# Performance work log

Measured on AMD Instinct MI355X. Metric: run time of the kernel, lower is better.

The kernel has to match this reference:

```python
import jax, jax.numpy as jnp
import numpy as np

M_CONST = 0.05  # monotonicity margin m from __init__ default


def setup_inputs() -> dict:
    key = jax.random.key(0)
    ks = jax.random.split(key, 5)
    B, IN, OUT = 262144, 128, 128
    scale = 1.0 / np.sqrt(IN)
    return {
        "x": jax.random.normal(ks[0], (B, IN), dtype=jnp.float32),
        "z": jax.random.normal(ks[1], (B, OUT), dtype=jnp.float32),
        "U_w": jax.random.normal(ks[2], (OUT, IN), dtype=jnp.float32) * scale,
        "U_b": jax.random.normal(ks[3], (OUT,), dtype=jnp.float32) * scale,
        "A_w": jax.random.normal(ks[4], (OUT, OUT), dtype=jnp.float32) * scale,
        "d": jnp.zeros((OUT,), dtype=jnp.float32),
    }


def reference(x, z, U_w, U_b, A_w, d):
    # U(x) = x @ U_w.T + U_b
    ux = x @ U_w.T + U_b
    # rowSums diag: diag(|A| @ 1) -> per-output-row abs row sums; z @ diag(r) = z * r
    row_sums = jnp.sum(jnp.abs(A_w), axis=1)  # [OUT]
    dw = jnp.exp(d)                            # diag weights
    # transformedA = diag(1/dw) @ A @ diag(dw); z @ transformedA.T = ((z*dw) @ A.T) * (1/dw)
    z_lin = ((z * dw) @ A_w.T) / dw
    z_out = M_CONST * z + z_lin - z * row_sums
    return (ux + z_out,)
```

## Files before the change

### kernel.cpp

```cpp
#include <hip/hip_runtime.h>
#include <hip/hip_bf16.h>

typedef __attribute__((ext_vector_type(4))) float  f4;
typedef __attribute__((ext_vector_type(4))) float  f32x4;
typedef __attribute__((ext_vector_type(8))) short  bf8;
typedef __attribute__((ext_vector_type(4))) short  s4;

__device__ __forceinline__ short f2bf(float f) {
    unsigned u = __builtin_bit_cast(unsigned, f);
    u += 0x7fff + ((u >> 16) & 1);
    return (short)(u >> 16);
}

__global__ void nemon_prep(const float* __restrict__ Uw,
                           const float* __restrict__ Aw,
                           const float* __restrict__ dvec,
                           short* __restrict__ pre)
{
    __shared__ float rs[128], dwv[128];
    const int tid = threadIdx.x;
    if (tid < 128) {
        float s = 0.f;
        #pragma unroll 8
        for (int k = 0; k < 128; ++k) s += fabsf(Aw[tid * 128 + k]);
        rs[tid]  = s;
        dwv[tid] = expf(dvec[tid]);
    }
    __syncthreads();
    for (int e = tid; e < 32768; e += 256) {
        const int j    = e & 7;
        const int lane = (e >> 3) & 63;
        const int tnt  = e >> 9;
        const int nt   = tnt & 7;
        const int t    = tnt >> 3;
        const int k    = t * 32 + (lane >> 4) * 8 + j;
        const int n    = nt * 16 + (lane & 15);
        float v;
        if (k < 128) {
            v = Uw[n * 128 + k];
        } else {
            const int k2 = k - 128;
            v = Aw[n * 128 + k2] * (dwv[k2] / dwv[n]);
            if (n == k2) v += 0.05f - rs[n];
        }
        pre[e] = f2bf(v);
    }
}

__global__ __launch_bounds__(256, 3) void nemon_main(
    const float* __restrict__ x,
    const float* __restrict__ z,
    const float* __restrict__ Ub,
    const short* __restrict__ pre,
    float* __restrict__ out,
    int ntiles)
{
    __shared__ char S[16384];
    const int tid  = threadIdx.x;
    const int wave = tid >> 6;
    const int lane = tid & 63;
    const int mrow = lane & 15;
    const int kgrp = lane >> 4;

    bf8 wreg[8][2];
    #pragma unroll
    for (int kt = 0; kt < 8; ++kt) {
        #pragma unroll
        for (int j = 0; j < 2; ++j)
            wreg[kt][j] = *(const bf8*)&pre[((kt * 8 + (2 * wave + j)) * 64 + lane) * 8];
    }
    const float ub0 = Ub[(2 * wave)     * 16 + mrow];
    const float ub1 = Ub[(2 * wave + 1) * 16 + mrow];

    for (int tile = blockIdx.x; tile < ntiles; tile += gridDim.x) {
        const long base = (long)tile * 4096;

        f4 xv[4], zv[4];
        #pragma unroll
        for (int i = 0; i < 4; ++i) xv[i] = *(const f4*)(x + base + (tid + i * 256) * 4);
        #pragma unroll
        for (int i = 0; i < 4; ++i) zv[i] = *(const f4*)(z + base + (tid + i * 256) * 4);

        __syncthreads();

        #pragma unroll
        for (int i = 0; i < 4; ++i) {
            const int c   = tid + i * 256;
            const int row = c >> 5;
            const int k2  = (c & 31) * 8;
            const int swz = (row & 7) << 4;
            s4 px = { f2bf(xv[i][0]), f2bf(xv[i][1]), f2bf(xv[i][2]), f2bf(xv[i][3]) };
            s4 pz = { f2bf(zv[i][0]), f2bf(zv[i][1]), f2bf(zv[i][2]), f2bf(zv[i][3]) };
            *(s4*)(S + row * 512 + ( k2         ^ swz)) = px;
            *(s4*)(S + row * 512 + ((k2 + 256)  ^ swz)) = pz;
        }
        __syncthreads();

        f32x4 acc[2][2];
        acc[0][0] = (f32x4){ub0, ub0, ub0, ub0};
        acc[1][0] = acc[0][0];
        acc[0][1] = (f32x4){ub1, ub1, ub1, ub1};
        acc[1][1] = acc[0][1];
        #pragma unroll
        for (int m2 = 0; m2 < 2; ++m2) {
            const int row   = m2 * 16 + mrow;
            const int rbase = row * 512;
            const int swz   = (row & 7) << 4;
            #pragma unroll
            for (int kt = 0; kt < 8; ++kt) {
                bf8 a = *(const bf8*)(S + rbase + ((kt * 64 + kgrp * 16) ^ swz));
                acc[m2][0] = __builtin_amdgcn_mfma_f32_16x16x32_bf16(a, wreg[kt][0], acc[m2][0], 0, 0, 0);
                acc[m2][1] = __builtin_amdgcn_mfma_f32_16x16x32_bf16(a, wreg[kt][1], acc[m2][1], 0, 0, 0);
            }
        }
        __syncthreads();

        float* SF = (float*)S;
        #pragma unroll
        for (int m2 = 0; m2 < 2; ++m2) {
            #pragma unroll
            for (int j2 = 0; j2 < 2; ++j2) {
                #pragma unroll
                for (int jj = 0; jj < 4; ++jj)
                    SF[(m2 * 16 + kgrp * 4 + jj) * 128 + (2 * wave + j2) * 16 + mrow] = acc[m2][j2][jj];
            }
        }
        __syncthreads();

        #pragma unroll
        for (int i = 0; i < 4; ++i) {
            f4 v = *(const f4*)(S + (tid + i * 256) * 16);
            *(f4*)(out + base + (tid + i * 256) * 4) = v;
        }
    }
}

extern "C" void kernel_launch(void* const* d_in, const int* in_sizes, int n_in,
                              void* d_out, int out_size, void* d_ws, size_t ws_size,
                              hipStream_t stream) {
    const float* x  = (const float*)d_in[0];
    const float* z  = (const float*)d_in[1];
    const float* Uw = (const float*)d_in[2];
    const float* Ub = (const float*)d_in[3];
    const float* Aw = (const float*)d_in[4];
    const float* dv = (const float*)d_in[5];
    float* out = (float*)d_out;
    short* pre = (short*)d_ws;

    const int B      = in_sizes[0] / 128;
    const int ntiles = B / 32;

    nemon_prep<<<1, 256, 0, stream>>>(Uw, Aw, dv, pre);
    nemon_main<<<2048, 256, 0, stream>>>(x, z, Ub, pre, out, ntiles);
}
```

Measured before the change: 120.3 us.

## Double-buffer input tiles, prefetch next tile, and swizzle output staging

Loads the next tile's x and z into registers while the current tile runs its MFMA work. The bf16 input goes into alternating LDS buffers and the output staging gets its own LDS region, which removes one barrier per iteration. Output staging writes and reads now use an XOR swizzle, meant to avoid LDS bank conflicts. LDS per block grows from 16KB to 48KB and the prefetch keeps more registers live, which may limit occupancy under the 3-blocks-per-CU launch bound.

```diff
diff --git a/kernel.cpp b/kernel.cpp
--- a/kernel.cpp
+++ b/kernel.cpp
@@ -55,12 +55,27 @@
     float* __restrict__ out,
     int ntiles)
 {
-    __shared__ char S[16384];
+    __shared__ char S[49152];
+    float* OF = (float*)(S + 32768);
+
     const int tid  = threadIdx.x;
     const int wave = tid >> 6;
     const int lane = tid & 63;
     const int mrow = lane & 15;
     const int kgrp = lane >> 4;
+
+    const int niter = (ntiles > (int)blockIdx.x)
+                    ? (ntiles - blockIdx.x + gridDim.x - 1) / gridDim.x : 0;
+    long base = (long)blockIdx.x * 4096;
+    const long bstride = (long)gridDim.x * 4096;
+
+    f4 xv[4], zv[4];
+    if (niter > 0) {
+        #pragma unroll
+        for (int i = 0; i < 4; ++i) xv[i] = *(const f4*)(x + base + (tid + i * 256) * 4);
+        #pragma unroll
+        for (int i = 0; i < 4; ++i) zv[i] = *(const f4*)(z + base + (tid + i * 256) * 4);
+    }
 
     bf8 wreg[8][2];
     #pragma unroll
@@ -72,16 +87,9 @@
     const float ub0 = Ub[(2 * wave)     * 16 + mrow];
     const float ub1 = Ub[(2 * wave + 1) * 16 + mrow];
 
-    for (int tile = blockIdx.x; tile < ntiles; tile += gridDim.x) {
-        const long base = (long)tile * 4096;
-
-        f4 xv[4], zv[4];
-        #pragma unroll
-        for (int i = 0; i < 4; ++i) xv[i] = *(const f4*)(x + base + (tid + i * 256) * 4);
-        #pragma unroll
-        for (int i = 0; i < 4; ++i) zv[i] = *(const f4*)(z + base + (tid + i * 256) * 4);
-
-        __syncthreads();
+    for (int it = 0; it < niter; ++it) {
+        char* inb = S + ((it & 1) << 14);
+        const long cur = base;
 
         #pragma unroll
         for (int i = 0; i < 4; ++i) {
@@ -91,10 +99,18 @@
             const int swz = (row & 7) << 4;
             s4 px = { f2bf(xv[i][0]), f2bf(xv[i][1]), f2bf(xv[i][2]), f2bf(xv[i][3]) };
             s4 pz = { f2bf(zv[i][0]), f2bf(zv[i][1]), f2bf(zv[i][2]), f2bf(zv[i][3]) };
-            *(s4*)(S + row * 512 + ( k2         ^ swz)) = px;
-            *(s4*)(S + row * 512 + ((k2 + 256)  ^ swz)) = pz;
+            *(s4*)(inb + row * 512 + ( k2        ^ swz)) = px;
+            *(s4*)(inb + row * 512 + ((k2 + 256) ^ swz)) = pz;
         }
         __syncthreads();
+
+        base += bstride;
+        if (it + 1 < niter) {
+            #pragma unroll
+            for (int i = 0; i < 4; ++i) xv[i] = *(const f4*)(x + base + (tid + i * 256) * 4);
+            #pragma unroll
+            for (int i = 0; i < 4; ++i) zv[i] = *(const f4*)(z + base + (tid + i * 256) * 4);
+        }
 
         f32x4 acc[2][2];
         acc[0][0] = (f32x4){ub0, ub0, ub0, ub0};
@@ -103,34 +119,37 @@
         acc[1][1] = acc[0][1];
         #pragma unroll
         for (int m2 = 0; m2 < 2; ++m2) {
-            const int row   = m2 * 16 + mrow;
-            const int rbase = row * 512;
-            const int swz   = (row & 7) << 4;
+            const int rbase = (m2 * 16 + mrow) * 512;
+            const int swz   = (mrow & 7) << 4;
             #pragma unroll
             for (int kt = 0; kt < 8; ++kt) {
-                bf8 a = *(const bf8*)(S + rbase + ((kt * 64 + kgrp * 16) ^ swz));
+                bf8 a = *(const bf8*)(inb + rbase + ((kt * 64 + kgrp * 16) ^ swz));
                 acc[m2][0] = __builtin_amdgcn_mfma_f32_16x16x32_bf16(a, wreg[kt][0], acc[m2][0], 0, 0, 0);
                 acc[m2][1] = __builtin_amdgcn_mfma_f32_16x16x32_bf16(a, wreg[kt][1], acc[m2][1], 0, 0, 0);
             }
         }
-        __syncthreads();
 
-        float* SF = (float*)S;
         #pragma unroll
         for (int m2 = 0; m2 < 2; ++m2) {
             #pragma unroll
             for (int j2 = 0; j2 < 2; ++j2) {
+                const int col  = (2 * wave + j2) * 16 + mrow;
+                const int cols = col ^ (kgrp << 2) ^ ((kgrp >> 1) << 4);
                 #pragma unroll
                 for (int jj = 0; jj < 4; ++jj)
-                    SF[(m2 * 16 + kgrp * 4 + jj) * 128 + (2 * wave + j2) * 16 + mrow] = acc[m2][j2][jj];
+                    OF[(m2 * 16 + kgrp * 4 + jj) * 128 + cols] = acc[m2][j2][jj];
             }
         }
         __syncthreads();
 
         #pragma unroll
         for (int i = 0; i < 4; ++i) {
-            f4 v = *(const f4*)(S + (tid + i * 256) * 16);
-            *(f4*)(out + base + (tid + i * 256) * 4) = v;
+            const int q = tid + i * 256;
+            const int r = q >> 5;
+            const int c = q & 31;
+            const int s = (r >> 2) & 3;
+            f4 v = *(const f4*)((char*)OF + r * 512 + (((c << 4) ^ (s << 4) ^ ((s >> 1) << 6))));
+            *(f4*)(out + cur + q * 4) = v;
         }
     }
 }
```

New measurement: 120.1 us. Within noise of the previous version (-0.2%).
